# Kernel optimization log

Measured on AMD Instinct MI355X. Metric: run time of the kernel, lower is better.

The kernel has to match this reference:

```python
import jax, jax.numpy as jnp
import numpy as np

N = 100000
E = 3200000
EPS = 1e-5


def setup_inputs() -> dict:
    key = jax.random.key(0)
    ks = jax.random.split(key, 6)
    x = jax.random.normal(ks[0], (N, 512), dtype=jnp.float32)
    edge_row = jax.random.randint(ks[1], (E,), 0, N, dtype=jnp.int32)
    edge_col = jax.random.randint(ks[2], (E,), 0, N, dtype=jnp.int32)
    edge_val = jax.random.uniform(ks[3], (E,), dtype=jnp.float32)
    W1 = jax.random.normal(ks[4], (512, 256), dtype=jnp.float32) * (1.0 / np.sqrt(512))
    W2 = jax.random.normal(ks[5], (256, 64), dtype=jnp.float32) * (1.0 / np.sqrt(256))
    gamma1 = jnp.ones((256,), jnp.float32)
    beta1 = jnp.zeros((256,), jnp.float32)
    gamma2 = jnp.ones((64,), jnp.float32)
    beta2 = jnp.zeros((64,), jnp.float32)
    return dict(x=x, edge_row=edge_row, edge_col=edge_col, edge_val=edge_val,
                W1=W1, gamma1=gamma1, beta1=beta1, W2=W2, gamma2=gamma2, beta2=beta2)


def spmm(row, col, val, dense):
    # out[i] = sum_{e: row[e]==i} val[e] * dense[col[e]]
    msgs = val[:, None] * dense[col]  # [E, F]
    return jax.ops.segment_sum(msgs, row, num_segments=N)


def batchnorm(h, gamma, beta):
    # BatchNorm1d in training mode: batch (node-dim) statistics, biased variance
    mean = jnp.mean(h, axis=0)
    var = jnp.var(h, axis=0)
    return (h - mean) * jax.lax.rsqrt(var + EPS) * gamma + beta


def reference(x, edge_row, edge_col, edge_val, W1, gamma1, beta1, W2, gamma2, beta2):
    # layer 1: dense GEMM -> sparse aggregate -> relu (GNNLayer active=True)
    h = spmm(edge_row, edge_col, edge_val, x @ W1)
    h = jax.nn.relu(h)
    h = batchnorm(h, gamma1, beta1)
    h = jax.nn.relu(h)
    # dropout treated as identity (inference mode) for deterministic reference
    h = spmm(edge_row, edge_col, edge_val, h @ W2)
    h = jax.nn.relu(h)
    h = batchnorm(h, gamma2, beta2)
    return h
```

## Files before the change

### kernel.cpp

```cpp
#include <hip/hip_runtime.h>

#define EPS 1e-5f

typedef __attribute__((ext_vector_type(8))) short short8;
typedef __attribute__((ext_vector_type(4))) float floatx4;
typedef __attribute__((ext_vector_type(4))) unsigned short ushortx4;
typedef __attribute__((ext_vector_type(2))) unsigned short ushortx2;

__device__ __forceinline__ unsigned short f2bf(float f) {
    unsigned u = __float_as_uint(f);
    unsigned r = (u + 0x7FFFu + ((u >> 16) & 1u)) >> 16;
    return (unsigned short)r;
}
__device__ __forceinline__ float bf2f(unsigned short h) {
    return __uint_as_float((unsigned)h << 16);
}

__global__ void zero_kernel(int* __restrict__ hist2, float* __restrict__ stats,
                            int n_hist, int n_stats) {
    int i = blockIdx.x * 256 + threadIdx.x;
    if (i < n_hist)  hist2[i] = 0;
    if (i < n_stats) stats[i] = 0.0f;
}

__global__ __launch_bounds__(256) void bucket_hist_kernel(const int* __restrict__ erow,
                                                          int* __restrict__ hist2,
                                                          int E, int chunk, int nb) {
    __shared__ int cnt[1024];
    int g = blockIdx.x & 7;
    for (int i = threadIdx.x; i < nb; i += 256) cnt[i] = 0;
    __syncthreads();
    int base = blockIdx.x * chunk;
    int end = min(base + chunk, E);
    for (int j = base + threadIdx.x; j < end; j += 256)
        atomicAdd(&cnt[erow[j] >> 7], 1);
    __syncthreads();
    for (int i = threadIdx.x; i < nb; i += 256) {
        int c = cnt[i];
        if (c) atomicAdd(&hist2[i * 8 + g], c);
    }
}

__global__ __launch_bounds__(1024) void bucket_scan_kernel(const int* __restrict__ hist2,
                                                           int* __restrict__ cursor2,
                                                           int* __restrict__ bucket_start,
                                                           int* __restrict__ row_start,
                                                           int nb, int n, int E) {
    __shared__ int lds[1024];
    int t = threadIdx.x;
    int total = nb * 8;
    int per = (total + 1023) >> 10;
    int s0 = t * per, s1 = min(s0 + per, total);
    int sum = 0;
    for (int i = s0; i < s1; i++) sum += hist2[i];
    lds[t] = sum;
    __syncthreads();
    for (int off = 1; off < 1024; off <<= 1) {
        int v = (t >= off) ? lds[t - off] : 0;
        __syncthreads();
        lds[t] += v;
        __syncthreads();
    }
    int run = lds[t] - sum;
    for (int i = s0; i < s1; i++) {
        cursor2[i] = run;
        if ((i & 7) == 0) bucket_start[i >> 3] = run;
        run += hist2[i];
    }
    if (t == 0) { bucket_start[nb] = E; row_start[n] = E; }
}

__global__ __launch_bounds__(256) void pass1_scatter_kernel(const int* __restrict__ erow,
                                                            const int* __restrict__ ecol,
                                                            const float* __restrict__ ev,
                                                            int* __restrict__ cursor2,
                                                            int2* __restrict__ tmp,
                                                            int E, int chunk) {
    int g = blockIdx.x & 7;
    int base = blockIdx.x * chunk;
    int end = min(base + chunk, E);
    for (int j = base + threadIdx.x; j < end; j += 256) {
        int r = erow[j];
        int b = r >> 7, lr = r & 127;
        int key = ecol[j] | (lr << 17);
        int p = atomicAdd(&cursor2[b * 8 + g], 1);
        tmp[p] = make_int2(key, __float_as_int(ev[j]));
    }
}

__global__ __launch_bounds__(256) void pass2_kernel(const int2* __restrict__ tmp,
                                                    const int* __restrict__ bucket_start,
                                                    int* __restrict__ row_start,
                                                    int2* __restrict__ edges, int n) {
    __shared__ int cnt[128], scn[128], cur[128];
    int b = blockIdx.x, t = threadIdx.x;
    int bstart = bucket_start[b], bend = bucket_start[b + 1];
    if (t < 128) cnt[t] = 0;
    __syncthreads();
    for (int j = bstart + t; j < bend; j += 256)
        atomicAdd(&cnt[((unsigned)tmp[j].x) >> 17], 1);
    __syncthreads();
    if (t < 128) scn[t] = cnt[t];
    __syncthreads();
#pragma unroll
    for (int off = 1; off < 128; off <<= 1) {
        int v = 0;
        if (t < 128 && t >= off) v = scn[t - off];
        __syncthreads();
        if (t < 128) scn[t] += v;
        __syncthreads();
    }
    if (t < 128) {
        int pref = scn[t] - cnt[t];
        cur[t] = pref;
        int r = b * 128 + t;
        if (r <= n) row_start[r] = bstart + pref;
    }
    __syncthreads();
    for (int j = bstart + t; j < bend; j += 256) {
        int2 e = tmp[j];
        int lr = ((unsigned)e.x) >> 17;
        int pos = atomicAdd(&cur[lr], 1);
        edges[bstart + pos] = make_int2(e.x & 0x1FFFF, e.y);
    }
}

__global__ void prep_w1_kernel(const float* __restrict__ W1,
                               unsigned short* __restrict__ Bhi,
                               unsigned short* __restrict__ Blo) {
    int idx = blockIdx.x * 256 + threadIdx.x;
    int nn = idx >> 9, k = idx & 511;
    float w = W1[(size_t)k * 256 + nn];
    unsigned short hi = f2bf(w);
    float rem = w - bf2f(hi);
    Bhi[idx] = hi;
    Blo[idx] = f2bf(rem);
}

__global__ __launch_bounds__(256) void gemm1_mfma_kernel(const float* __restrict__ A,
                                                         const unsigned short* __restrict__ Bhi,
                                                         const unsigned short* __restrict__ Blo,
                                                         unsigned short* __restrict__ H0, int M) {
    __shared__ unsigned short AsH[128][32];
    __shared__ unsigned short AsL[128][32];
    __shared__ unsigned short BsH[128][32];
    __shared__ unsigned short BsL[128][32];
    int tid  = threadIdx.x;
    int lane = tid & 63, w = tid >> 6;
    int wm = w & 1, wn = w >> 1;
    int rowBase = blockIdx.y * 128;
    int colBase = blockIdx.x * 128;

    floatx4 acc[4][4];
#pragma unroll
    for (int i = 0; i < 4; i++)
#pragma unroll
        for (int j = 0; j < 4; j++)
#pragma unroll
            for (int r = 0; r < 4; r++) acc[i][j][r] = 0.0f;

    int r    = tid >> 1;
    int half = tid & 1;
    bool aval = (rowBase + r) < M;
    const float* aptr = A + (size_t)(rowBase + r) * 512 + half * 16;
    const unsigned short* bhptr = Bhi + (size_t)(colBase + r) * 512 + half * 16;
    const unsigned short* blptr = Blo + (size_t)(colBase + r) * 512 + half * 16;

    int cl = lane & 15, quad = lane >> 4;
    int q8 = quad * 8;

    for (int k0 = 0; k0 < 512; k0 += 32) {
        float f[16];
        if (aval) {
            *(float4*)&f[0]  = *(const float4*)(aptr + k0);
            *(float4*)&f[4]  = *(const float4*)(aptr + k0 + 4);
            *(float4*)&f[8]  = *(const float4*)(aptr + k0 + 8);
            *(float4*)&f[12] = *(const float4*)(aptr + k0 + 12);
        } else {
#pragma unroll
            for (int t = 0; t < 16; t++) f[t] = 0.0f;
        }
        union { unsigned short s[16]; uint4 q[2]; } ph, pl;
#pragma unroll
        for (int t = 0; t < 16; t++) {
            unsigned short hi = f2bf(f[t]);
            ph.s[t] = hi;
            pl.s[t] = f2bf(f[t] - bf2f(hi));
        }
        *(uint4*)&AsH[r][half * 16]     = ph.q[0];
        *(uint4*)&AsH[r][half * 16 + 8] = ph.q[1];
        *(uint4*)&AsL[r][half * 16]     = pl.q[0];
        *(uint4*)&AsL[r][half * 16 + 8] = pl.q[1];
        *(uint4*)&BsH[r][half * 16]     = *(const uint4*)(bhptr + k0);
        *(uint4*)&BsH[r][half * 16 + 8] = *(const uint4*)(bhptr + k0 + 8);
        *(uint4*)&BsL[r][half * 16]     = *(const uint4*)(blptr + k0);
        *(uint4*)&BsL[r][half * 16 + 8] = *(const uint4*)(blptr + k0 + 8);
        __syncthreads();

        short8 ah[4], al[4], bh[4], bl[4];
#pragma unroll
        for (int mt = 0; mt < 4; mt++) {
            ah[mt] = *(short8*)&AsH[wm * 64 + mt * 16 + cl][q8];
            al[mt] = *(short8*)&AsL[wm * 64 + mt * 16 + cl][q8];
        }
#pragma unroll
        for (int nt = 0; nt < 4; nt++) {
            bh[nt] = *(short8*)&BsH[wn * 64 + nt * 16 + cl][q8];
            bl[nt] = *(short8*)&BsL[wn * 64 + nt * 16 + cl][q8];
        }
#pragma unroll
        for (int mt = 0; mt < 4; mt++)
#pragma unroll
            for (int nt = 0; nt < 4; nt++) {
                acc[mt][nt] = __builtin_amdgcn_mfma_f32_16x16x32_bf16(ah[mt], bh[nt], acc[mt][nt], 0, 0, 0);
                acc[mt][nt] = __builtin_amdgcn_mfma_f32_16x16x32_bf16(al[mt], bh[nt], acc[mt][nt], 0, 0, 0);
                acc[mt][nt] = __builtin_amdgcn_mfma_f32_16x16x32_bf16(ah[mt], bl[nt], acc[mt][nt], 0, 0, 0);
            }
        __syncthreads();
    }

#pragma unroll
    for (int mt = 0; mt < 4; mt++) {
#pragma unroll
        for (int reg = 0; reg < 4; reg++) {
            int gr = rowBase + wm * 64 + mt * 16 + quad * 4 + reg;
            if (gr < M) {
#pragma unroll
                for (int nt = 0; nt < 4; nt++) {
                    H0[(size_t)gr * 256 + colBase + wn * 64 + nt * 16 + cl] = f2bf(acc[mt][nt][reg]);
                }
            }
        }
    }
}

__global__ __launch_bounds__(256) void agg1_kernel(const unsigned short* __restrict__ H0,
                                                   const int* __restrict__ rs,
                                                   const int2* __restrict__ edges,
                                                   float* __restrict__ H1, int n) {
    int w = threadIdx.x >> 6, lane = threadIdx.x & 63;
    int i = blockIdx.x * 4 + w;
    if (i >= n) return;
    int start = rs[i], end = rs[i + 1];
    int fo = lane << 2;
    float4 acc = make_float4(0.f, 0.f, 0.f, 0.f);
    int j = start;
    for (; j + 8 <= end; j += 8) {
        int2 e[8];
        ushortx4 u[8];
#pragma unroll
        for (int t = 0; t < 8; t++) e[t] = edges[j + t];
#pragma unroll
        for (int t = 0; t < 8; t++)
            u[t] = *(const ushortx4*)(H0 + (size_t)e[t].x * 256 + fo);
#pragma unroll
        for (int t = 0; t < 8; t++) {
            float v = __int_as_float(e[t].y);
            acc.x += v * bf2f(u[t].x);
            acc.y += v * bf2f(u[t].y);
            acc.z += v * bf2f(u[t].z);
            acc.w += v * bf2f(u[t].w);
        }
    }
    for (; j < end; j++) {
        int2 e = edges[j];
        float v = __int_as_float(e.y);
        ushortx4 u = *(const ushortx4*)(H0 + (size_t)e.x * 256 + fo);
        acc.x += v * bf2f(u.x);
        acc.y += v * bf2f(u.y);
        acc.z += v * bf2f(u.z);
        acc.w += v * bf2f(u.w);
    }
    float4 o;
    o.x = fmaxf(acc.x, 0.f); o.y = fmaxf(acc.y, 0.f);
    o.z = fmaxf(acc.z, 0.f); o.w = fmaxf(acc.w, 0.f);
    *(float4*)(H1 + (size_t)i * 256 + fo) = o;
}

__global__ __launch_bounds__(256) void colstats1_kernel(const float* __restrict__ H1,
                                                        float* __restrict__ sums,
                                                        float* __restrict__ sumsq,
                                                        int n, int rpb) {
    int tid = threadIdx.x;
    int r0 = blockIdx.x * rpb;
    int r1 = min(r0 + rpb, n);
    float s = 0.f, q = 0.f;
    for (int rr = r0; rr < r1; rr++) {
        float v = H1[(size_t)rr * 256 + tid];
        s += v; q += v * v;
    }
    atomicAdd(&sums[tid], s);
    atomicAdd(&sumsq[tid], q);
}

__global__ void bnparams_kernel(const float* __restrict__ sums, const float* __restrict__ sumsq,
                                const float* __restrict__ gamma, const float* __restrict__ beta,
                                float* __restrict__ scale, float* __restrict__ shift,
                                int C, float invN) {
    int c = threadIdx.x;
    if (c < C) {
        float mean = sums[c] * invN;
        float var  = sumsq[c] * invN - mean * mean;
        float rstd = rsqrtf(var + EPS);
        float sc   = gamma[c] * rstd;
        scale[c] = sc;
        shift[c] = beta[c] - mean * sc;
    }
}

__global__ __launch_bounds__(256) void gemm2_kernel(const float* __restrict__ H1,
                                                    const float* __restrict__ W2,
                                                    const float* __restrict__ scale1,
                                                    const float* __restrict__ shift1,
                                                    unsigned short* __restrict__ H2, int M) {
    __shared__ float As[8][129];
    __shared__ float Bs[8][64];
    int tid = threadIdx.x;
    int tx = tid & 15, ty = tid >> 4;
    int rowBase = blockIdx.x * 128;
    float acc[8][4];
#pragma unroll
    for (int i = 0; i < 8; i++)
#pragma unroll
        for (int j = 0; j < 4; j++) acc[i][j] = 0.0f;

    int r   = tid >> 1;
    int kq  = (tid & 1) * 4;
    int bkk = tid >> 6;
    int bcol = tid & 63;

    for (int k0 = 0; k0 < 256; k0 += 8) {
        float4 a4 = make_float4(0.f, 0.f, 0.f, 0.f);
        int arow = rowBase + r;
        if (arow < M) a4 = *(const float4*)(H1 + (size_t)arow * 256 + k0 + kq);
        float av[4] = {a4.x, a4.y, a4.z, a4.w};
#pragma unroll
        for (int jj = 0; jj < 4; jj++) {
            int kk = k0 + kq + jj;
            float t = av[jj] * scale1[kk] + shift1[kk];
            As[kq + jj][r] = fmaxf(t, 0.0f);
        }
        Bs[bkk][bcol]     = W2[(size_t)(k0 + bkk) * 64 + bcol];
        Bs[bkk + 4][bcol] = W2[(size_t)(k0 + bkk + 4) * 64 + bcol];
        __syncthreads();
#pragma unroll
        for (int k = 0; k < 8; k++) {
            float ra[8], rb[4];
#pragma unroll
            for (int i = 0; i < 8; i++) ra[i] = As[k][ty * 8 + i];
#pragma unroll
            for (int j = 0; j < 4; j++) rb[j] = Bs[k][tx * 4 + j];
#pragma unroll
            for (int i = 0; i < 8; i++)
#pragma unroll
                for (int j = 0; j < 4; j++) acc[i][j] += ra[i] * rb[j];
        }
        __syncthreads();
    }
#pragma unroll
    for (int i = 0; i < 8; i++) {
        int crow = rowBase + ty * 8 + i;
        if (crow < M) {
            ushortx4 o;
            o.x = f2bf(acc[i][0]); o.y = f2bf(acc[i][1]);
            o.z = f2bf(acc[i][2]); o.w = f2bf(acc[i][3]);
            *(ushortx4*)(H2 + (size_t)crow * 64 + tx * 4) = o;
        }
    }
}

__global__ __launch_bounds__(256) void agg2_kernel(const unsigned short* __restrict__ H2,
                                                   const int* __restrict__ rs,
                                                   const int2* __restrict__ edges,
                                                   float* __restrict__ H3, int n) {
    int w = threadIdx.x >> 6, lane = threadIdx.x & 63;
    int half = lane >> 5, sub = lane & 31;
    int i = blockIdx.x * 8 + w * 2 + half;
    if (i >= n) return;
    int start = rs[i], end = rs[i + 1];
    int fo = sub << 1;
    float accx = 0.f, accy = 0.f;
    int j = start;
    for (; j + 4 <= end; j += 4) {
        int2 e[4];
        ushortx2 u[4];
#pragma unroll
        for (int t = 0; t < 4; t++) e[t] = edges[j + t];
#pragma unroll
        for (int t = 0; t < 4; t++)
            u[t] = *(const ushortx2*)(H2 + (size_t)e[t].x * 64 + fo);
#pragma unroll
        for (int t = 0; t < 4; t++) {
            float v = __int_as_float(e[t].y);
            accx += v * bf2f(u[t].x);
            accy += v * bf2f(u[t].y);
        }
    }
    for (; j < end; j++) {
        int2 e = edges[j];
        float v = __int_as_float(e.y);
        ushortx2 u = *(const ushortx2*)(H2 + (size_t)e.x * 64 + fo);
        accx += v * bf2f(u.x);
        accy += v * bf2f(u.y);
    }
    float2 o;
    o.x = fmaxf(accx, 0.f);
    o.y = fmaxf(accy, 0.f);
    *(float2*)(H3 + (size_t)i * 64 + fo) = o;
}

__global__ __launch_bounds__(256) void colstats2_kernel(const float* __restrict__ H3,
                                                        float* __restrict__ sums,
                                                        float* __restrict__ sumsq,
                                                        int n, int rpb) {
    int c = threadIdx.x & 63, rsub = threadIdx.x >> 6;
    int base = blockIdx.x * rpb;
    int r1 = min(base + rpb, n);
    float s = 0.f, q = 0.f;
    for (int rr = base + rsub; rr < r1; rr += 4) {
        float v = H3[(size_t)rr * 64 + c];
        s += v; q += v * v;
    }
    atomicAdd(&sums[c], s);
    atomicAdd(&sumsq[c], q);
}

__global__ void bnapply_kernel(float* __restrict__ out, const float* __restrict__ scale,
                               const float* __restrict__ shift, int total) {
    int idx = blockIdx.x * 256 + threadIdx.x;
    if (idx < total) {
        int c = idx & 63;
        out[idx] = out[idx] * scale[c] + shift[c];
    }
}

extern "C" void kernel_launch(void* const* d_in, const int* in_sizes, int n_in,
                              void* d_out, int out_size, void* d_ws, size_t ws_size,
                              hipStream_t stream) {
    const float* x    = (const float*)d_in[0];
    const int*   erow = (const int*)d_in[1];
    const int*   ecol = (const int*)d_in[2];
    const float* ev   = (const float*)d_in[3];
    const float* W1   = (const float*)d_in[4];
    const float* g1   = (const float*)d_in[5];
    const float* b1   = (const float*)d_in[6];
    const float* W2   = (const float*)d_in[7];
    const float* g2   = (const float*)d_in[8];
    const float* b2   = (const float*)d_in[9];
    float* out = (float*)d_out;

    int n = in_sizes[0] / 512;
    int E = in_sizes[1];
    int nb = (n + 127) >> 7;
    int chunk = 16384;
    int nchunks = (E + chunk - 1) / chunk;

    char* ws = (char*)d_ws;
    size_t off = 0;
    auto alloc = [&](size_t bytes) { size_t o = off; off += (bytes + 255) & ~(size_t)255; return o; };

    int*   hist2        = (int*)(ws + alloc((size_t)nb * 8 * 4));
    int*   cursor2      = (int*)(ws + alloc((size_t)nb * 8 * 4));
    int*   bucket_start = (int*)(ws + alloc((size_t)(nb + 1) * 4));
    int*   row_start    = (int*)(ws + alloc((size_t)(n + 1) * 4));
    int2*  tmp          = (int2*)(ws + alloc((size_t)E * 8));
    int2*  edges        = (int2*)(ws + alloc((size_t)E * 8));
    unsigned short* h0  = (unsigned short*)(ws + alloc((size_t)n * 256 * 2));
    float* h1           = (float*)(ws + alloc((size_t)n * 256 * 4));
    unsigned short* h2  = (unsigned short*)(ws + alloc((size_t)n * 64 * 2));
    unsigned short* w1hi = (unsigned short*)(ws + alloc((size_t)256 * 512 * 2));
    unsigned short* w1lo = (unsigned short*)(ws + alloc((size_t)256 * 512 * 2));
    float* stats        = (float*)(ws + alloc(2048 * 4));
    float* sums1  = stats;
    float* sumsq1 = stats + 256;
    float* sums2  = stats + 512;
    float* sumsq2 = stats + 576;
    float* scale1 = stats + 640;
    float* shift1 = stats + 896;
    float* scale2 = stats + 1152;
    float* shift2 = stats + 1216;

    float invN = 1.0f / (float)n;

    zero_kernel<<<dim3((nb * 8 + 255) / 256), dim3(256), 0, stream>>>(hist2, stats, nb * 8, 640);
    bucket_hist_kernel<<<dim3(nchunks), dim3(256), 0, stream>>>(erow, hist2, E, chunk, nb);
    bucket_scan_kernel<<<dim3(1), dim3(1024), 0, stream>>>(hist2, cursor2, bucket_start, row_start, nb, n, E);
    pass1_scatter_kernel<<<dim3(nchunks), dim3(256), 0, stream>>>(erow, ecol, ev, cursor2, tmp, E, chunk);
    pass2_kernel<<<dim3(nb), dim3(256), 0, stream>>>(tmp, bucket_start, row_start, edges, n);
    prep_w1_kernel<<<dim3(512), dim3(256), 0, stream>>>(W1, w1hi, w1lo);
    gemm1_mfma_kernel<<<dim3(2, (n + 127) / 128), dim3(256), 0, stream>>>(x, w1hi, w1lo, h0, n);
    agg1_kernel<<<dim3((n + 3) / 4), dim3(256), 0, stream>>>(h0, row_start, edges, h1, n);
    colstats1_kernel<<<dim3(400), dim3(256), 0, stream>>>(h1, sums1, sumsq1, n, (n + 399) / 400);
    bnparams_kernel<<<dim3(1), dim3(256), 0, stream>>>(sums1, sumsq1, g1, b1, scale1, shift1, 256, invN);
    gemm2_kernel<<<dim3((n + 127) / 128), dim3(256), 0, stream>>>(h1, W2, scale1, shift1, h2, n);
    agg2_kernel<<<dim3((n + 7) / 8), dim3(256), 0, stream>>>(h2, row_start, edges, out, n);
    colstats2_kernel<<<dim3(200), dim3(256), 0, stream>>>(out, sums2, sumsq2, n, (n + 199) / 200);
    bnparams_kernel<<<dim3(1), dim3(64), 0, stream>>>(sums2, sumsq2, g2, b2, scale2, shift2, 64, invN);
    bnapply_kernel<<<dim3((n * 64 + 255) / 256), dim3(256), 0, stream>>>(out, scale2, shift2, n * 64);

    (void)n_in; (void)out_size; (void)ws_size;
}
```

Baseline: 1.093 ms.

## Use MFMA for second GEMM, store H1 in bf16, widen GEMM1 tile to full N

The scalar FP32 gemm2 is replaced by an MFMA bf16 kernel that uses a hi/lo split of W2 and applies batchnorm and relu while loading A. The intermediate H1 is stored as bf16 instead of fp32, which halves its write and read traffic in agg1, colstats1 and gemm2. GEMM1 now computes all 256 output columns per block, so x is read and converted once instead of twice, at the cost of more registers and LDS and launch_bounds(256,1). H1 loses precision from bf16 rounding, and the A operand of GEMM2 is no longer hi/lo split.

```diff
diff --git a/kernel.cpp b/kernel.cpp
--- a/kernel.cpp
+++ b/kernel.cpp
@@ -132,30 +132,39 @@
     int nn = idx >> 9, k = idx & 511;
     float w = W1[(size_t)k * 256 + nn];
     unsigned short hi = f2bf(w);
-    float rem = w - bf2f(hi);
     Bhi[idx] = hi;
-    Blo[idx] = f2bf(rem);
-}
-
-__global__ __launch_bounds__(256) void gemm1_mfma_kernel(const float* __restrict__ A,
-                                                         const unsigned short* __restrict__ Bhi,
-                                                         const unsigned short* __restrict__ Blo,
-                                                         unsigned short* __restrict__ H0, int M) {
+    Blo[idx] = f2bf(w - bf2f(hi));
+}
+
+__global__ void prep_w2_kernel(const float* __restrict__ W2,
+                               unsigned short* __restrict__ Bhi,
+                               unsigned short* __restrict__ Blo) {
+    int idx = blockIdx.x * 256 + threadIdx.x;
+    int nn = idx >> 8, k = idx & 255;
+    float w = W2[(size_t)k * 64 + nn];
+    unsigned short hi = f2bf(w);
+    Bhi[idx] = hi;
+    Blo[idx] = f2bf(w - bf2f(hi));
+}
+
+__global__ __launch_bounds__(256, 1) void gemm1_mfma_kernel(const float* __restrict__ A,
+                                                            const unsigned short* __restrict__ Bhi,
+                                                            const unsigned short* __restrict__ Blo,
+                                                            unsigned short* __restrict__ H0, int M) {
     __shared__ unsigned short AsH[128][32];
     __shared__ unsigned short AsL[128][32];
-    __shared__ unsigned short BsH[128][32];
-    __shared__ unsigned short BsL[128][32];
+    __shared__ unsigned short BsH[256][32];
+    __shared__ unsigned short BsL[256][32];
     int tid  = threadIdx.x;
     int lane = tid & 63, w = tid >> 6;
     int wm = w & 1, wn = w >> 1;
-    int rowBase = blockIdx.y * 128;
-    int colBase = blockIdx.x * 128;
-
-    floatx4 acc[4][4];
+    int rowBase = blockIdx.x * 128;
+
+    floatx4 acc[4][8];
 #pragma unroll
     for (int i = 0; i < 4; i++)
 #pragma unroll
-        for (int j = 0; j < 4; j++)
+        for (int j = 0; j < 8; j++)
 #pragma unroll
             for (int r = 0; r < 4; r++) acc[i][j][r] = 0.0f;
 
@@ -163,8 +172,8 @@
     int half = tid & 1;
     bool aval = (rowBase + r) < M;
     const float* aptr = A + (size_t)(rowBase + r) * 512 + half * 16;
-    const unsigned short* bhptr = Bhi + (size_t)(colBase + r) * 512 + half * 16;
-    const unsigned short* blptr = Blo + (size_t)(colBase + r) * 512 + half * 16;
+    const unsigned short* bhptr = Bhi + (size_t)tid * 512;
+    const unsigned short* blptr = Blo + (size_t)tid * 512;
 
     int cl = lane & 15, quad = lane >> 4;
     int q8 = quad * 8;
@@ -191,31 +200,33 @@
         *(uint4*)&AsH[r][half * 16 + 8] = ph.q[1];
         *(uint4*)&AsL[r][half * 16]     = pl.q[0];
         *(uint4*)&AsL[r][half * 16 + 8] = pl.q[1];
-        *(uint4*)&BsH[r][half * 16]     = *(const uint4*)(bhptr + k0);
-        *(uint4*)&BsH[r][half * 16 + 8] = *(const uint4*)(bhptr + k0 + 8);
-        *(uint4*)&BsL[r][half * 16]     = *(const uint4*)(blptr + k0);
-        *(uint4*)&BsL[r][half * 16 + 8] = *(const uint4*)(blptr + k0 + 8);
-        __syncthreads();
-
-        short8 ah[4], al[4], bh[4], bl[4];
+        *(uint4*)&BsH[tid][0]  = *(const uint4*)(bhptr + k0);
+        *(uint4*)&BsH[tid][8]  = *(const uint4*)(bhptr + k0 + 8);
+        *(uint4*)&BsH[tid][16] = *(const uint4*)(bhptr + k0 + 16);
+        *(uint4*)&BsH[tid][24] = *(const uint4*)(bhptr + k0 + 24);
+        *(uint4*)&BsL[tid][0]  = *(const uint4*)(blptr + k0);
+        *(uint4*)&BsL[tid][8]  = *(const uint4*)(blptr + k0 + 8);
+        *(uint4*)&BsL[tid][16] = *(const uint4*)(blptr + k0 + 16);
+        *(uint4*)&BsL[tid][24] = *(const uint4*)(blptr + k0 + 24);
+        __syncthreads();
+
+        short8 ah[4], al[4];
 #pragma unroll
         for (int mt = 0; mt < 4; mt++) {
             ah[mt] = *(short8*)&AsH[wm * 64 + mt * 16 + cl][q8];
             al[mt] = *(short8*)&AsL[wm * 64 + mt * 16 + cl][q8];
         }
 #pragma unroll
-        for (int nt = 0; nt < 4; nt++) {
-            bh[nt] = *(short8*)&BsH[wn * 64 + nt * 16 + cl][q8];
-            bl[nt] = *(short8*)&BsL[wn * 64 + nt * 16 + cl][q8];
-        }
-#pragma unroll
-        for (int mt = 0; mt < 4; mt++)
-#pragma unroll
-            for (int nt = 0; nt < 4; nt++) {
-                acc[mt][nt] = __builtin_amdgcn_mfma_f32_16x16x32_bf16(ah[mt], bh[nt], acc[mt][nt], 0, 0, 0);
-                acc[mt][nt] = __builtin_amdgcn_mfma_f32_16x16x32_bf16(al[mt], bh[nt], acc[mt][nt], 0, 0, 0);
-                acc[mt][nt] = __builtin_amdgcn_mfma_f32_16x16x32_bf16(ah[mt], bl[nt], acc[mt][nt], 0, 0, 0);
+        for (int nt = 0; nt < 8; nt++) {
+            short8 bh = *(short8*)&BsH[wn * 128 + nt * 16 + cl][q8];
+            short8 bl = *(short8*)&BsL[wn * 128 + nt * 16 + cl][q8];
+#pragma unroll
+            for (int mt = 0; mt < 4; mt++) {
+                acc[mt][nt] = __builtin_amdgcn_mfma_f32_16x16x32_bf16(ah[mt], bh, acc[mt][nt], 0, 0, 0);
+                acc[mt][nt] = __builtin_amdgcn_mfma_f32_16x16x32_bf16(al[mt], bh, acc[mt][nt], 0, 0, 0);
+                acc[mt][nt] = __builtin_amdgcn_mfma_f32_16x16x32_bf16(ah[mt], bl, acc[mt][nt], 0, 0, 0);
             }
+        }
         __syncthreads();
     }
 
@@ -226,8 +237,8 @@
             int gr = rowBase + wm * 64 + mt * 16 + quad * 4 + reg;
             if (gr < M) {
 #pragma unroll
-                for (int nt = 0; nt < 4; nt++) {
-                    H0[(size_t)gr * 256 + colBase + wn * 64 + nt * 16 + cl] = f2bf(acc[mt][nt][reg]);
+                for (int nt = 0; nt < 8; nt++) {
+                    H0[(size_t)gr * 256 + wn * 128 + nt * 16 + cl] = f2bf(acc[mt][nt][reg]);
                 }
             }
         }
@@ -237,7 +248,7 @@
 __global__ __launch_bounds__(256) void agg1_kernel(const unsigned short* __restrict__ H0,
                                                    const int* __restrict__ rs,
                                                    const int2* __restrict__ edges,
-                                                   float* __restrict__ H1, int n) {
+                                                   unsigned short* __restrict__ H1, int n) {
     int w = threadIdx.x >> 6, lane = threadIdx.x & 63;
     int i = blockIdx.x * 4 + w;
     if (i >= n) return;
@@ -271,13 +282,13 @@
         acc.z += v * bf2f(u.z);
         acc.w += v * bf2f(u.w);
     }
-    float4 o;
-    o.x = fmaxf(acc.x, 0.f); o.y = fmaxf(acc.y, 0.f);
-    o.z = fmaxf(acc.z, 0.f); o.w = fmaxf(acc.w, 0.f);
-    *(float4*)(H1 + (size_t)i * 256 + fo) = o;
-}
-
-__global__ __launch_bounds__(256) void colstats1_kernel(const float* __restrict__ H1,
+    ushortx4 o;
+    o.x = f2bf(fmaxf(acc.x, 0.f)); o.y = f2bf(fmaxf(acc.y, 0.f));
+    o.z = f2bf(fmaxf(acc.z, 0.f)); o.w = f2bf(fmaxf(acc.w, 0.f));
+    *(ushortx4*)(H1 + (size_t)i * 256 + fo) = o;
+}
+
+__global__ __launch_bounds__(256) void colstats1_kernel(const unsigned short* __restrict__ H1,
                                                         float* __restrict__ sums,
                                                         float* __restrict__ sumsq,
                                                         int n, int rpb) {
@@ -286,7 +297,7 @@
     int r1 = min(r0 + rpb, n);
     float s = 0.f, q = 0.f;
     for (int rr = r0; rr < r1; rr++) {
-        float v = H1[(size_t)rr * 256 + tid];
+        float v = bf2f(H1[(size_t)rr * 256 + tid]);
         s += v; q += v * v;
     }
     atomicAdd(&sums[tid], s);
@@ -308,63 +319,106 @@
     }
 }
 
-__global__ __launch_bounds__(256) void gemm2_kernel(const float* __restrict__ H1,
-                                                    const float* __restrict__ W2,
-                                                    const float* __restrict__ scale1,
-                                                    const float* __restrict__ shift1,
-                                                    unsigned short* __restrict__ H2, int M) {
-    __shared__ float As[8][129];
-    __shared__ float Bs[8][64];
-    int tid = threadIdx.x;
-    int tx = tid & 15, ty = tid >> 4;
+__global__ __launch_bounds__(256) void gemm2_mfma_kernel(const unsigned short* __restrict__ H1,
+                                                         const unsigned short* __restrict__ Bhi,
+                                                         const unsigned short* __restrict__ Blo,
+                                                         const float* __restrict__ scale1,
+                                                         const float* __restrict__ shift1,
+                                                         unsigned short* __restrict__ H2, int M) {
+    __shared__ unsigned short As[128][32];
+    __shared__ unsigned short BsH[64][32];
+    __shared__ unsigned short BsL[64][32];
+    int tid  = threadIdx.x;
+    int lane = tid & 63, w = tid >> 6;
+    int wm = w & 1, wn = w >> 1;
     int rowBase = blockIdx.x * 128;
-    float acc[8][4];
-#pragma unroll
-    for (int i = 0; i < 8; i++)
-#pragma unroll
-        for (int j = 0; j < 4; j++) acc[i][j] = 0.0f;
-
-    int r   = tid >> 1;
-    int kq  = (tid & 1) * 4;
-    int bkk = tid >> 6;
-    int bcol = tid & 63;
-
-    for (int k0 = 0; k0 < 256; k0 += 8) {
-        float4 a4 = make_float4(0.f, 0.f, 0.f, 0.f);
-        int arow = rowBase + r;
-        if (arow < M) a4 = *(const float4*)(H1 + (size_t)arow * 256 + k0 + kq);
-        float av[4] = {a4.x, a4.y, a4.z, a4.w};
-#pragma unroll
-        for (int jj = 0; jj < 4; jj++) {
-            int kk = k0 + kq + jj;
-            float t = av[jj] * scale1[kk] + shift1[kk];
-            As[kq + jj][r] = fmaxf(t, 0.0f);
-        }
-        Bs[bkk][bcol]     = W2[(size_t)(k0 + bkk) * 64 + bcol];
-        Bs[bkk + 4][bcol] = W2[(size_t)(k0 + bkk + 4) * 64 + bcol];
-        __syncthreads();
-#pragma unroll
-        for (int k = 0; k < 8; k++) {
-            float ra[8], rb[4];
-#pragma unroll
-            for (int i = 0; i < 8; i++) ra[i] = As[k][ty * 8 + i];
-#pragma unroll
-            for (int j = 0; j < 4; j++) rb[j] = Bs[k][tx * 4 + j];
-#pragma unroll
-            for (int i = 0; i < 8; i++)
-#pragma unroll
-                for (int j = 0; j < 4; j++) acc[i][j] += ra[i] * rb[j];
-        }
-        __syncthreads();
-    }
-#pragma unroll
-    for (int i = 0; i < 8; i++) {
-        int crow = rowBase + ty * 8 + i;
-        if (crow < M) {
-            ushortx4 o;
-            o.x = f2bf(acc[i][0]); o.y = f2bf(acc[i][1]);
-            o.z = f2bf(acc[i][2]); o.w = f2bf(acc[i][3]);
-            *(ushortx4*)(H2 + (size_t)crow * 64 + tx * 4) = o;
+
+    floatx4 acc[4][2];
+#pragma unroll
+    for (int i = 0; i < 4; i++)
+#pragma unroll
+        for (int j = 0; j < 2; j++)
+#pragma unroll
+            for (int r = 0; r < 4; r++) acc[i][j][r] = 0.0f;
+
+    int r    = tid >> 1;
+    int half = tid & 1;
+    bool aval = (rowBase + r) < M;
+    const unsigned short* aptr = H1 + (size_t)(rowBase + r) * 256 + half * 16;
+
+    int cl = lane & 15, quad = lane >> 4;
+    int q8 = quad * 8;
+
+    for (int k0 = 0; k0 < 256; k0 += 32) {
+        union { unsigned short s[16]; uint4 q[2]; } pa;
+        if (aval) {
+            uint4 u0 = *(const uint4*)(aptr + k0);
+            uint4 u1 = *(const uint4*)(aptr + k0 + 8);
+            unsigned short raw[16];
+            *(uint4*)&raw[0] = u0;
+            *(uint4*)&raw[8] = u1;
+            int kb = k0 + half * 16;
+            float4 sc0 = *(const float4*)(scale1 + kb);
+            float4 sc1 = *(const float4*)(scale1 + kb + 4);
+            float4 sc2 = *(const float4*)(scale1 + kb + 8);
+            float4 sc3 = *(const float4*)(scale1 + kb + 12);
+            float4 sh0 = *(const float4*)(shift1 + kb);
+            float4 sh1 = *(const float4*)(shift1 + kb + 4);
+            float4 sh2 = *(const float4*)(shift1 + kb + 8);
+            float4 sh3 = *(const float4*)(shift1 + kb + 12);
+            float scv[16] = {sc0.x, sc0.y, sc0.z, sc0.w, sc1.x, sc1.y, sc1.z, sc1.w,
+                             sc2.x, sc2.y, sc2.z, sc2.w, sc3.x, sc3.y, sc3.z, sc3.w};
+            float shv[16] = {sh0.x, sh0.y, sh0.z, sh0.w, sh1.x, sh1.y, sh1.z, sh1.w,
+                             sh2.x, sh2.y, sh2.z, sh2.w, sh3.x, sh3.y, sh3.z, sh3.w};
+#pragma unroll
+            for (int t = 0; t < 16; t++) {
+                float vv = bf2f(raw[t]) * scv[t] + shv[t];
+                pa.s[t] = f2bf(fmaxf(vv, 0.0f));
+            }
+        } else {
+#pragma unroll
+            for (int t = 0; t < 16; t++) pa.s[t] = 0;
+        }
+        *(uint4*)&As[r][half * 16]     = pa.q[0];
+        *(uint4*)&As[r][half * 16 + 8] = pa.q[1];
+        if (tid < 128) {
+            int row = tid & 63;
+            const unsigned short* bp = ((tid < 64) ? Bhi : Blo) + (size_t)row * 256;
+            unsigned short (*bs)[32] = (tid < 64) ? BsH : BsL;
+            *(uint4*)&bs[row][0]  = *(const uint4*)(bp + k0);
+            *(uint4*)&bs[row][8]  = *(const uint4*)(bp + k0 + 8);
+            *(uint4*)&bs[row][16] = *(const uint4*)(bp + k0 + 16);
+            *(uint4*)&bs[row][24] = *(const uint4*)(bp + k0 + 24);
+        }
+        __syncthreads();
+
+        short8 af[4];
+#pragma unroll
+        for (int mt = 0; mt < 4; mt++) af[mt] = *(short8*)&As[wm * 64 + mt * 16 + cl][q8];
+#pragma unroll
+        for (int nt = 0; nt < 2; nt++) {
+            short8 bh = *(short8*)&BsH[wn * 32 + nt * 16 + cl][q8];
+            short8 bl = *(short8*)&BsL[wn * 32 + nt * 16 + cl][q8];
+#pragma unroll
+            for (int mt = 0; mt < 4; mt++) {
+                acc[mt][nt] = __builtin_amdgcn_mfma_f32_16x16x32_bf16(af[mt], bh, acc[mt][nt], 0, 0, 0);
+                acc[mt][nt] = __builtin_amdgcn_mfma_f32_16x16x32_bf16(af[mt], bl, acc[mt][nt], 0, 0, 0);
+            }
+        }
+        __syncthreads();
+    }
+
+#pragma unroll
+    for (int mt = 0; mt < 4; mt++) {
+#pragma unroll
+        for (int reg = 0; reg < 4; reg++) {
+            int gr = rowBase + wm * 64 + mt * 16 + quad * 4 + reg;
+            if (gr < M) {
+#pragma unroll
+                for (int nt = 0; nt < 2; nt++) {
+                    H2[(size_t)gr * 64 + wn * 32 + nt * 16 + cl] = f2bf(acc[mt][nt][reg]);
+                }
+            }
         }
     }
 }
@@ -466,10 +520,12 @@
     int2*  tmp          = (int2*)(ws + alloc((size_t)E * 8));
     int2*  edges        = (int2*)(ws + alloc((size_t)E * 8));
     unsigned short* h0  = (unsigned short*)(ws + alloc((size_t)n * 256 * 2));
-    float* h1           = (float*)(ws + alloc((size_t)n * 256 * 4));
+    unsigned short* h1  = (unsigned short*)(ws + alloc((size_t)n * 256 * 2));
     unsigned short* h2  = (unsigned short*)(ws + alloc((size_t)n * 64 * 2));
     unsigned short* w1hi = (unsigned short*)(ws + alloc((size_t)256 * 512 * 2));
     unsigned short* w1lo = (unsigned short*)(ws + alloc((size_t)256 * 512 * 2));
+    unsigned short* w2hi = (unsigned short*)(ws + alloc((size_t)64 * 256 * 2));
+    unsigned short* w2lo = (unsigned short*)(ws + alloc((size_t)64 * 256 * 2));
     float* stats        = (float*)(ws + alloc(2048 * 4));
     float* sums1  = stats;
     float* sumsq1 = stats + 256;
@@ -488,11 +544,12 @@
     pass1_scatter_kernel<<<dim3(nchunks), dim3(256), 0, stream>>>(erow, ecol, ev, cursor2, tmp, E, chunk);
     pass2_kernel<<<dim3(nb), dim3(256), 0, stream>>>(tmp, bucket_start, row_start, edges, n);
     prep_w1_kernel<<<dim3(512), dim3(256), 0, stream>>>(W1, w1hi, w1lo);
-    gemm1_mfma_kernel<<<dim3(2, (n + 127) / 128), dim3(256), 0, stream>>>(x, w1hi, w1lo, h0, n);
+    prep_w2_kernel<<<dim3(64), dim3(256), 0, stream>>>(W2, w2hi, w2lo);
+    gemm1_mfma_kernel<<<dim3((n + 127) / 128), dim3(256), 0, stream>>>(x, w1hi, w1lo, h0, n);
     agg1_kernel<<<dim3((n + 3) / 4), dim3(256), 0, stream>>>(h0, row_start, edges, h1, n);
     colstats1_kernel<<<dim3(400), dim3(256), 0, stream>>>(h1, sums1, sumsq1, n, (n + 399) / 400);
     bnparams_kernel<<<dim3(1), dim3(256), 0, stream>>>(sums1, sumsq1, g1, b1, scale1, shift1, 256, invN);
-    gemm2_kernel<<<dim3((n + 127) / 128), dim3(256), 0, stream>>>(h1, W2, scale1, shift1, h2, n);
+    gemm2_mfma_kernel<<<dim3((n + 127) / 128), dim3(256), 0, stream>>>(h1, w2hi, w2lo, scale1, shift1, h2, n);
     agg2_kernel<<<dim3((n + 7) / 8), dim3(256), 0, stream>>>(h2, row_start, edges, out, n);
     colstats2_kernel<<<dim3(200), dim3(256), 0, stream>>>(out, sums2, sumsq2, n, (n + 199) / 200);
     bnparams_kernel<<<dim3(1), dim3(64), 0, stream>>>(sums2, sumsq2, g2, b2, scale2, shift2, 64, invN);
```

Result: no change. 1.105 ms (+1.0%).
